# Optimization experiments

Hardware: AMD Instinct MI355X
Metric: run time of the kernel (lower is better)

Reference implementation:

```python
import jax, jax.numpy as jnp
import numpy as np

D_MODEL = 1024
D_STATE = 16
D_CONV = 4
EXPAND = 2
MLP_EXPAND = 2
D_INNER = EXPAND * D_MODEL          # 2048
DT_RANK = (D_MODEL + 15) // 16      # 64
BATCH, SEQ = 2, 1024


def setup_inputs() -> dict:
    key = jax.random.key(0)
    ks = jax.random.split(key, 16)
    s = 0.02
    inp = {
        "x": jax.random.normal(ks[0], (BATCH, SEQ, D_MODEL), jnp.float32),
        "norm1_g": jnp.ones((D_MODEL,), jnp.float32),
        "norm1_b": jnp.zeros((D_MODEL,), jnp.float32),
        "in_proj_w": jax.random.normal(ks[1], (2 * D_INNER, D_MODEL), jnp.float32) * s,
        "conv_w": jax.random.normal(ks[2], (D_INNER, 1, D_CONV), jnp.float32) * s,
        "conv_b": jnp.zeros((D_INNER,), jnp.float32),
        "x_proj_w": jax.random.normal(ks[3], (DT_RANK + 2 * D_STATE, D_INNER), jnp.float32) * s,
        "dt_proj_w": jax.random.normal(ks[4], (D_INNER, DT_RANK), jnp.float32) * s,
        "dt_proj_b": jax.random.normal(ks[5], (D_INNER,), jnp.float32) * 0.1,
        "A_log": jnp.log(jnp.broadcast_to(jnp.arange(1, D_STATE + 1, dtype=jnp.float32), (D_INNER, D_STATE))),
        "D_param": jnp.ones((D_INNER,), jnp.float32),
        "out_proj_w": jax.random.normal(ks[6], (D_MODEL, D_INNER), jnp.float32) * s,
        "norm2_g": jnp.ones((D_MODEL,), jnp.float32),
        "norm2_b": jnp.zeros((D_MODEL,), jnp.float32),
        "mlp_w1": jax.random.normal(ks[7], (MLP_EXPAND * D_MODEL, D_MODEL), jnp.float32) * s,
        "mlp_b1": jnp.zeros((MLP_EXPAND * D_MODEL,), jnp.float32),
        "mlp_w2": jax.random.normal(ks[8], (D_MODEL, MLP_EXPAND * D_MODEL), jnp.float32) * s,
        "mlp_b2": jnp.zeros((D_MODEL,), jnp.float32),
    }
    return inp


def _layernorm(x, g, b, eps=1e-5):
    m = jnp.mean(x, axis=-1, keepdims=True)
    v = jnp.var(x, axis=-1, keepdims=True)
    return (x - m) * jax.lax.rsqrt(v + eps) * g + b


def _silu(x):
    return x * jax.nn.sigmoid(x)


def _mamba(x, in_proj_w, conv_w, conv_b, x_proj_w, dt_proj_w, dt_proj_b, A_log, D_param, out_proj_w):
    # x: (B, L, d_model)
    xz = x @ in_proj_w.T                              # (B, L, 2*Di)
    xc, z = jnp.split(xz, 2, axis=-1)                 # each (B, L, Di)
    # causal depthwise conv over time
    xc_t = xc.transpose(0, 2, 1)                      # (B, Di, L)
    xc_t = jax.lax.conv_general_dilated(
        xc_t, conv_w, window_strides=(1,), padding=[(D_CONV - 1, 0)],
        dimension_numbers=("NCH", "OIH", "NCH"), feature_group_count=D_INNER,
    ) + conv_b[None, :, None]
    xc = _silu(xc_t).transpose(0, 2, 1)               # (B, L, Di)

    dbc = xc @ x_proj_w.T                             # (B, L, dt_rank + 2N)
    dt, Bm, Cm = jnp.split(dbc, [DT_RANK, DT_RANK + D_STATE], axis=-1)
    dt = jax.nn.softplus(dt @ dt_proj_w.T + dt_proj_b)  # (B, L, Di)
    A = -jnp.exp(A_log)                               # (Di, N)

    def step(h, inp):
        dt_t, B_t, C_t, x_t = inp                     # (B,Di),(B,N),(B,N),(B,Di)
        dA = jnp.exp(dt_t[..., None] * A)             # (B, Di, N)
        h = dA * h + (dt_t * x_t)[..., None] * B_t[:, None, :]
        y = jnp.einsum("bdn,bn->bd", h, C_t)
        return h, y

    h0 = jnp.zeros((x.shape[0], D_INNER, D_STATE), x.dtype)
    xs = (dt.transpose(1, 0, 2), Bm.transpose(1, 0, 2), Cm.transpose(1, 0, 2), xc.transpose(1, 0, 2))
    _, ys = jax.lax.scan(step, h0, xs)                # ys: (L, B, Di)
    y = ys.transpose(1, 0, 2) + xc * D_param          # skip term D*x
    y = y * _silu(z)
    return y @ out_proj_w.T                           # (B, L, d_model)


def reference(x, norm1_g, norm1_b, in_proj_w, conv_w, conv_b, x_proj_w, dt_proj_w,
              dt_proj_b, A_log, D_param, out_proj_w, norm2_g, norm2_b,
              mlp_w1, mlp_b1, mlp_w2, mlp_b2):
    # residual + Mamba(LN(x))  (droppath=0 -> identity)
    h = x + _mamba(_layernorm(x, norm1_g, norm1_b), in_proj_w, conv_w, conv_b,
                   x_proj_w, dt_proj_w, dt_proj_b, A_log, D_param, out_proj_w)
    # residual + MLP(LN(h))    (dropout eval -> identity)
    m = _layernorm(h, norm2_g, norm2_b)
    m = jax.nn.gelu(m @ mlp_w1.T + mlp_b1, approximate=False) @ mlp_w2.T + mlp_b2
    return h + m
```

## Files before the change

### kernel.cpp

```cpp
#include <hip/hip_runtime.h>
#include <math.h>

#define D_MODEL 1024
#define D_INNER 2048
#define DT_RANK 64
#define D_STATE 16
#define NBC 96
#define BATCH 2
#define SEQ 1024
#define TOK (BATCH*SEQ)
#define CS 32
#define NCH 32
#define XKSPLIT 16

typedef __attribute__((ext_vector_type(8))) short short8;
typedef __attribute__((ext_vector_type(4))) float f32x4;
typedef __attribute__((ext_vector_type(4))) unsigned short us4;

__device__ __forceinline__ float softplus_f(float x) {
    return (x > 20.0f) ? x : log1pf(__expf(x));
}
__device__ __forceinline__ float gelu_f(float x) {
    return 0.5f * x * (1.0f + erff(x * 0.70710678118654752f));
}
__device__ __forceinline__ float silu_f(float x) {
    return x / (1.0f + __expf(-x));
}
__device__ __forceinline__ ushort f2bf(float f) {
    unsigned u = __float_as_uint(f);
    unsigned r = (u + 0x7fffu + ((u >> 16) & 1u)) >> 16;
    return (ushort)r;
}
__device__ __forceinline__ float bf2f(ushort u) {
    return __uint_as_float(((unsigned)u) << 16);
}

__global__ void prep_kernel(const float* __restrict__ x, const float* __restrict__ g,
                            const float* __restrict__ b, ushort* __restrict__ ln_out,
                            const float* __restrict__ Wp, const float* __restrict__ Wo,
                            const float* __restrict__ W1, const float* __restrict__ W2,
                            const float* __restrict__ Wx, const float* __restrict__ Wdt,
                            ushort* __restrict__ Wpb, ushort* __restrict__ Wob,
                            ushort* __restrict__ W1b, ushort* __restrict__ W2b,
                            ushort* __restrict__ Wxb, ushort* __restrict__ Wdtb) {
    int tid = threadIdx.x;
    if (blockIdx.x < TOK) {
        int row = blockIdx.x;
        const float* xr = x + (size_t)row * D_MODEL;
        ushort* outr = ln_out + (size_t)row * D_MODEL;
        float4 v = ((const float4*)xr)[tid];
        float s  = v.x + v.y + v.z + v.w;
        float sq = v.x*v.x + v.y*v.y + v.z*v.z + v.w*v.w;
        #pragma unroll
        for (int o = 32; o > 0; o >>= 1) {
            s  += __shfl_down(s,  o);
            sq += __shfl_down(sq, o);
        }
        __shared__ float ss[4], ssq[4];
        int wid = tid >> 6, lane = tid & 63;
        if (lane == 0) { ss[wid] = s; ssq[wid] = sq; }
        __syncthreads();
        if (tid == 0) {
            float a = 0.f, c = 0.f;
            for (int i = 0; i < 4; i++) { a += ss[i]; c += ssq[i]; }
            ss[0] = a; ssq[0] = c;
        }
        __syncthreads();
        float mean = ss[0] * (1.0f / D_MODEL);
        float var  = ssq[0] * (1.0f / D_MODEL) - mean * mean;
        float rstd = rsqrtf(var + 1e-5f);
        float4 gg = ((const float4*)g)[tid];
        float4 bb = ((const float4*)b)[tid];
        ushort4 o;
        o.x = f2bf((v.x - mean) * rstd * gg.x + bb.x);
        o.y = f2bf((v.y - mean) * rstd * gg.y + bb.y);
        o.z = f2bf((v.z - mean) * rstd * gg.z + bb.z);
        o.w = f2bf((v.w - mean) * rstd * gg.w + bb.w);
        ((ushort4*)outr)[tid] = o;
        return;
    }
    int i = (blockIdx.x - TOK) * 256 + tid;
    const float* src; ushort* dst; int off;
    if      (i < 1048576) { src = Wp;  dst = Wpb;  off = i; }
    else if (i < 1572864) { src = Wo;  dst = Wob;  off = i - 1048576; }
    else if (i < 2097152) { src = W1;  dst = W1b;  off = i - 1572864; }
    else if (i < 2621440) { src = W2;  dst = W2b;  off = i - 2097152; }
    else if (i < 2670592) { src = Wx;  dst = Wxb;  off = i - 2621440; }
    else if (i < 2703360) { src = Wdt; dst = Wdtb; off = i - 2670592; }
    else return;
    float4 v = ((const float4*)src)[off];
    ushort4 o;
    o.x = f2bf(v.x); o.y = f2bf(v.y); o.z = f2bf(v.z); o.w = f2bf(v.w);
    ((ushort4*)dst)[off] = o;
}

__global__ void ln_bf16_kernel(const float* __restrict__ x, const float* __restrict__ g,
                               const float* __restrict__ b, ushort* __restrict__ out) {
    int row = blockIdx.x;
    const float* xr = x + (size_t)row * D_MODEL;
    ushort* outr = out + (size_t)row * D_MODEL;
    int tid = threadIdx.x;
    float4 v = ((const float4*)xr)[tid];
    float s  = v.x + v.y + v.z + v.w;
    float sq = v.x*v.x + v.y*v.y + v.z*v.z + v.w*v.w;
    #pragma unroll
    for (int o = 32; o > 0; o >>= 1) {
        s  += __shfl_down(s,  o);
        sq += __shfl_down(sq, o);
    }
    __shared__ float ss[4], ssq[4];
    int wid = tid >> 6, lane = tid & 63;
    if (lane == 0) { ss[wid] = s; ssq[wid] = sq; }
    __syncthreads();
    if (tid == 0) {
        float a = 0.f, c = 0.f;
        for (int i = 0; i < 4; i++) { a += ss[i]; c += ssq[i]; }
        ss[0] = a; ssq[0] = c;
    }
    __syncthreads();
    float mean = ss[0] * (1.0f / D_MODEL);
    float var  = ssq[0] * (1.0f / D_MODEL) - mean * mean;
    float rstd = rsqrtf(var + 1e-5f);
    float4 gg = ((const float4*)g)[tid];
    float4 bb = ((const float4*)b)[tid];
    ushort4 o;
    o.x = f2bf((v.x - mean) * rstd * gg.x + bb.x);
    o.y = f2bf((v.y - mean) * rstd * gg.y + bb.y);
    o.z = f2bf((v.z - mean) * rstd * gg.z + bb.z);
    o.w = f2bf((v.w - mean) * rstd * gg.w + bb.w);
    ((ushort4*)outr)[tid] = o;
}

template<int BM, int BN, int ACT, bool BIAS, bool RES, bool OUTBF>
__global__ __launch_bounds__(256)
void mfma_gemm(const ushort* __restrict__ A, const ushort* __restrict__ W,
               const float* __restrict__ bias,
               const float* __restrict__ res, int ldr,
               void* __restrict__ Cout, int ldc, int K) {
    constexpr int WM = BM / 2, WN = BN / 2, FM = WM / 16, FN = WN / 16;
    __shared__ __align__(16) ushort As[2][BM * 32];
    __shared__ __align__(16) ushort Ws[2][BN * 32];
    const int tid  = threadIdx.x;
    const int lane = tid & 63, w = tid >> 6;
    const int wr = w >> 1, wc = w & 1;
    const int row0 = blockIdx.y * BM, col0 = blockIdx.x * BN;
    const int l16 = lane >> 4, l15 = lane & 15;
    const int srow = tid >> 2;
    const int scol = (tid & 3) * 8;
    const int nk = K / 32;

    f32x4 acc[FM][FN] = {};

    auto stage = [&](int kk, int buf) {
        const int k0 = kk * 32;
        #pragma unroll
        for (int s = 0; s < BM / 64; s++) {
            const ushort* g = A + (size_t)(row0 + s * 64 + srow) * K + k0 + scol;
            __builtin_amdgcn_global_load_lds(
                (const __attribute__((address_space(1))) void*)g,
                (__attribute__((address_space(3))) void*)((char*)&As[buf][0] + s * 4096 + w * 1024),
                16, 0, 0);
        }
        #pragma unroll
        for (int s = 0; s < BN / 64; s++) {
            const ushort* g = W + (size_t)(col0 + s * 64 + srow) * K + k0 + scol;
            __builtin_amdgcn_global_load_lds(
                (const __attribute__((address_space(1))) void*)g,
                (__attribute__((address_space(3))) void*)((char*)&Ws[buf][0] + s * 4096 + w * 1024),
                16, 0, 0);
        }
    };

    stage(0, 0);
    __syncthreads();

    for (int kk = 0; kk < nk; kk++) {
        const int cur = kk & 1;
        if (kk + 1 < nk) stage(kk + 1, cur ^ 1);

        short8 a[FM], b[FN];
        #pragma unroll
        for (int m = 0; m < FM; m++)
            a[m] = *(const short8*)(&As[cur][0] + (wr * WM + m * 16 + l15) * 32 + l16 * 8);
        #pragma unroll
        for (int n = 0; n < FN; n++)
            b[n] = *(const short8*)(&Ws[cur][0] + (wc * WN + n * 16 + l15) * 32 + l16 * 8);
        #pragma unroll
        for (int m = 0; m < FM; m++)
            #pragma unroll
            for (int n = 0; n < FN; n++)
                acc[m][n] = __builtin_amdgcn_mfma_f32_16x16x32_bf16(a[m], b[n], acc[m][n], 0, 0, 0);
        __syncthreads();
    }

    #pragma unroll
    for (int m = 0; m < FM; m++) {
        const int r0 = row0 + wr * WM + m * 16 + l16 * 4;
        #pragma unroll
        for (int n = 0; n < FN; n++) {
            const int c = col0 + wc * WN + n * 16 + l15;
            const float bv = BIAS ? bias[c] : 0.f;
            #pragma unroll
            for (int q = 0; q < 4; q++) {
                const int r = r0 + q;
                float v = acc[m][n][q] + bv;
                if (ACT == 1) v = softplus_f(v);
                else if (ACT == 2) v = gelu_f(v);
                if (RES) v += res[(size_t)r * ldr + c];
                if (OUTBF) ((ushort*)Cout)[(size_t)r * ldc + c] = f2bf(v);
                else       ((float*)Cout)[(size_t)r * ldc + c] = v;
            }
        }
    }
}

__global__ __launch_bounds__(256)
void xproj_split_kernel(const ushort* __restrict__ A,
                        const ushort* __restrict__ W,
                        float* __restrict__ part) {
    __shared__ __align__(16) ushort As[2][128 * 64];
    __shared__ __align__(16) ushort Bs[2][96 * 64];
    const int tid = threadIdx.x;
    const int lane = tid & 63, w = tid >> 6;
    const int l16 = lane >> 4, l15 = lane & 15;
    const int kbase = blockIdx.x * (D_INNER / XKSPLIT);
    const int row0 = blockIdx.y * 128;
    const int srow = tid >> 3;
    const int scol = (tid & 7) * 8;

    f32x4 acc[2][6] = {};

    auto stage = [&](int k0, int buf) {
        #pragma unroll
        for (int s = 0; s < 4; s++) {
            const ushort* g = A + (size_t)(row0 + s * 32 + srow) * D_INNER + kbase + k0 + scol;
            __builtin_amdgcn_global_load_lds(
                (const __attribute__((address_space(1))) void*)g,
                (__attribute__((address_space(3))) void*)((char*)&As[buf][0] + s * 4096 + w * 1024),
                16, 0, 0);
        }
        #pragma unroll
        for (int s = 0; s < 3; s++) {
            const ushort* g = W + (size_t)(s * 32 + srow) * D_INNER + kbase + k0 + scol;
            __builtin_amdgcn_global_load_lds(
                (const __attribute__((address_space(1))) void*)g,
                (__attribute__((address_space(3))) void*)((char*)&Bs[buf][0] + s * 4096 + w * 1024),
                16, 0, 0);
        }
    };

    stage(0, 0);
    __syncthreads();

    const int nk = (D_INNER / XKSPLIT) / 64;
    for (int kk = 0; kk < nk; kk++) {
        const int cur = kk & 1;
        if (kk + 1 < nk) stage((kk + 1) * 64, cur ^ 1);
        #pragma unroll
        for (int ks = 0; ks < 2; ks++) {
            short8 a[2], b[6];
            #pragma unroll
            for (int m = 0; m < 2; m++)
                a[m] = *(const short8*)(&As[cur][0] + (w * 32 + m * 16 + l15) * 64 + ks * 32 + l16 * 8);
            #pragma unroll
            for (int n = 0; n < 6; n++)
                b[n] = *(const short8*)(&Bs[cur][0] + (n * 16 + l15) * 64 + ks * 32 + l16 * 8);
            #pragma unroll
            for (int m = 0; m < 2; m++)
                #pragma unroll
                for (int n = 0; n < 6; n++)
                    acc[m][n] = __builtin_amdgcn_mfma_f32_16x16x32_bf16(a[m], b[n], acc[m][n], 0, 0, 0);
        }
        __syncthreads();
    }

    float* p = part + (size_t)blockIdx.x * D_INNER * NBC;
    #pragma unroll
    for (int m = 0; m < 2; m++) {
        const int r0 = row0 + w * 32 + m * 16 + l16 * 4;
        #pragma unroll
        for (int n = 0; n < 6; n++) {
            const int c = n * 16 + l15;
            #pragma unroll
            for (int q = 0; q < 4; q++)
                p[(size_t)(r0 + q) * NBC + c] = acc[m][n][q];
        }
    }
}

__global__ void xproj_reduce_kernel(const float* __restrict__ part,
                                    float* __restrict__ dbc, ushort* __restrict__ dtin_b) {
    int i = blockIdx.x * 256 + threadIdx.x;
    if (i >= D_INNER * NBC) return;
    float s = 0.f;
    #pragma unroll
    for (int k = 0; k < XKSPLIT; k++) s += part[(size_t)k * D_INNER * NBC + i];
    dbc[i] = s;
    int r = i / NBC, c = i - r * NBC;
    if (c < DT_RANK) dtin_b[r * DT_RANK + c] = f2bf(s);
}

__global__ void conv_silu_kernel(const ushort* __restrict__ xzb, const float* __restrict__ cw,
                                 const float* __restrict__ cb, ushort* __restrict__ xcb) {
    int idx = blockIdx.x * 256 + threadIdx.x;
    int c  = idx & (D_INNER - 1);
    int bt = idx >> 11;
    int b  = bt >> 10;
    int t  = bt & (SEQ - 1);
    float acc = cb[c];
    #pragma unroll
    for (int j = 0; j < 4; j++) {
        int tt = t - 3 + j;
        if (tt >= 0) acc += cw[c*4 + j] * bf2f(xzb[((size_t)(b*SEQ + tt)) * 4096 + c]);
    }
    xcb[idx] = f2bf(silu_f(acc));
}

__global__ __launch_bounds__(256)
void scan_chunk_kernel(const ushort* __restrict__ dtb, const float* __restrict__ dbc,
                       const ushort* __restrict__ xcb, const float* __restrict__ A_log,
                       float* __restrict__ chunkA, float* __restrict__ chunkH) {
    __shared__ ushort dtS[64][36];
    __shared__ ushort xS[64][36];
    __shared__ float  BS[16][36];
    const int bid = blockIdx.x;
    const int dg = bid & 31, cc = (bid >> 5) & 31, b = bid >> 10;
    const int d0 = dg * 64;
    const int tid = threadIdx.x, lane = tid & 63, wv = tid >> 6;
    const int rbase = b * SEQ + cc * CS;

    #pragma unroll
    for (int k = 0; k < 8; k++) {
        int tt = k * 4 + wv;
        size_t row = (size_t)(rbase + tt);
        dtS[lane][tt] = dtb[row * D_INNER + d0 + lane];
        xS[lane][tt]  = xcb[row * D_INNER + d0 + lane];
    }
    #pragma unroll
    for (int k = 0; k < 2; k++) {
        int ii = k * 256 + tid;
        int val = ii & 15, tt = ii >> 4;
        BS[val][tt] = dbc[(size_t)(rbase + tt) * NBC + DT_RANK + val];
    }
    __syncthreads();

    const int d_local = tid >> 2, ng = tid & 3, nb = ng * 4;
    const int d = d0 + d_local;
    float Arow[4];
    #pragma unroll
    for (int j = 0; j < 4; j++) Arow[j] = -__expf(A_log[d * D_STATE + nb + j]);
    float h[4] = {};
    float ap[4] = {1.f, 1.f, 1.f, 1.f};
    #pragma unroll
    for (int it = 0; it < 8; ++it) {
        us4 dtu = *(const us4*)&dtS[d_local][it * 4];
        us4 xu  = *(const us4*)&xS[d_local][it * 4];
        f32x4 Bv[4];
        #pragma unroll
        for (int j = 0; j < 4; j++) Bv[j] = *(const f32x4*)&BS[nb + j][it * 4];
        #pragma unroll
        for (int q = 0; q < 4; ++q) {
            float dtv = bf2f(dtu[q]);
            float dtx = dtv * bf2f(xu[q]);
            #pragma unroll
            for (int j = 0; j < 4; j++) {
                float dA = __expf(dtv * Arow[j]);
                ap[j] *= dA;
                h[j] = dA * h[j] + dtx * Bv[j][q];
            }
        }
    }
    size_t obase = ((size_t)((b * NCH + cc) * D_INNER) + d) * D_STATE + nb;
    f32x4 av, hv;
    #pragma unroll
    for (int j = 0; j < 4; j++) { av[j] = ap[j]; hv[j] = h[j]; }
    *(f32x4*)&chunkA[obase] = av;
    *(f32x4*)&chunkH[obase] = hv;
}

__global__ __launch_bounds__(256)
void scan_final_kernel(const ushort* __restrict__ dtb, const float* __restrict__ dbc,
                       const ushort* __restrict__ xcb, const float* __restrict__ A_log,
                       const float* __restrict__ chunkA, const float* __restrict__ chunkH,
                       const ushort* __restrict__ xzb,
                       const float* __restrict__ Dp, ushort* __restrict__ yb) {
    __shared__ ushort dtS[64][36];
    __shared__ ushort xS[64][36];
    __shared__ ushort zS[64][36];
    __shared__ float  BS[16][36];
    __shared__ float  CSld[16][36];
    __shared__ ushort ySt[64][36];
    const int bid = blockIdx.x;
    const int dg = bid & 31, cc = (bid >> 5) & 31, b = bid >> 10;
    const int d0 = dg * 64;
    const int tid = threadIdx.x, lane = tid & 63, wv = tid >> 6;
    const int rbase = b * SEQ + cc * CS;

    #pragma unroll
    for (int k = 0; k < 8; k++) {
        int tt = k * 4 + wv;
        size_t row = (size_t)(rbase + tt);
        dtS[lane][tt] = dtb[row * D_INNER + d0 + lane];
        xS[lane][tt]  = xcb[row * D_INNER + d0 + lane];
        zS[lane][tt]  = xzb[row * 4096 + 2048 + d0 + lane];
    }
    #pragma unroll
    for (int k = 0; k < 4; k++) {
        int ii = k * 256 + tid;
        int val = ii & 31, tt = ii >> 5;
        float v = dbc[(size_t)(rbase + tt) * NBC + DT_RANK + val];
        if (val < 16) BS[val][tt] = v;
        else          CSld[val - 16][tt] = v;
    }

    const int d_local = tid >> 2, ng = tid & 3, nb = ng * 4;
    const int d = d0 + d_local;

    f32x4 hv = {0.f, 0.f, 0.f, 0.f};
    #pragma unroll 4
    for (int c = 0; c < cc; ++c) {
        size_t off = ((size_t)((b * NCH + c) * D_INNER) + d) * D_STATE + nb;
        f32x4 a  = *(const f32x4*)&chunkA[off];
        f32x4 hl = *(const f32x4*)&chunkH[off];
        hv = a * hv + hl;
    }
    float Arow[4];
    #pragma unroll
    for (int j = 0; j < 4; j++) Arow[j] = -__expf(A_log[d * D_STATE + nb + j]);
    float h[4];
    #pragma unroll
    for (int j = 0; j < 4; j++) h[j] = hv[j];
    const float Dpv = Dp[d];
    __syncthreads();

    #pragma unroll
    for (int it = 0; it < 8; ++it) {
        us4 dtu = *(const us4*)&dtS[d_local][it * 4];
        us4 xu  = *(const us4*)&xS[d_local][it * 4];
        f32x4 Bv[4], Cv[4];
        #pragma unroll
        for (int j = 0; j < 4; j++) {
            Bv[j] = *(const f32x4*)&BS[nb + j][it * 4];
            Cv[j] = *(const f32x4*)&CSld[nb + j][it * 4];
        }
        float yv4[4];
        #pragma unroll
        for (int q = 0; q < 4; ++q) {
            float dtv = bf2f(dtu[q]);
            float dtx = dtv * bf2f(xu[q]);
            float yv = 0.f;
            #pragma unroll
            for (int j = 0; j < 4; j++) {
                float dA = __expf(dtv * Arow[j]);
                h[j] = dA * h[j] + dtx * Bv[j][q];
                yv += h[j] * Cv[j][q];
            }
            yv4[q] = yv;
        }
        #pragma unroll
        for (int q = 0; q < 4; ++q) {
            yv4[q] += __shfl_xor(yv4[q], 1);
            yv4[q] += __shfl_xor(yv4[q], 2);
        }
        if (ng == 0) {
            us4 zu = *(const us4*)&zS[d_local][it * 4];
            us4 xo = *(const us4*)&xS[d_local][it * 4];
            us4 o;
            #pragma unroll
            for (int q = 0; q < 4; ++q) {
                float z = bf2f(zu[q]);
                o[q] = f2bf((yv4[q] + bf2f(xo[q]) * Dpv) * silu_f(z));
            }
            *(us4*)&ySt[d_local][it * 4] = o;
        }
    }
    __syncthreads();
    #pragma unroll
    for (int k = 0; k < 8; k++) {
        int tt = k * 4 + wv;
        yb[(size_t)(rbase + tt) * D_INNER + d0 + lane] = ySt[lane][tt];
    }
}

extern "C" void kernel_launch(void* const* d_in, const int* in_sizes, int n_in,
                              void* d_out, int out_size, void* d_ws, size_t ws_size,
                              hipStream_t stream) {
    const float* x    = (const float*)d_in[0];
    const float* n1g  = (const float*)d_in[1];
    const float* n1b  = (const float*)d_in[2];
    const float* Wp   = (const float*)d_in[3];
    const float* cw   = (const float*)d_in[4];
    const float* cb   = (const float*)d_in[5];
    const float* Wx   = (const float*)d_in[6];
    const float* Wdt  = (const float*)d_in[7];
    const float* bdt  = (const float*)d_in[8];
    const float* Alog = (const float*)d_in[9];
    const float* Dp   = (const float*)d_in[10];
    const float* Wo   = (const float*)d_in[11];
    const float* n2g  = (const float*)d_in[12];
    const float* n2b  = (const float*)d_in[13];
    const float* W1   = (const float*)d_in[14];
    const float* b1   = (const float*)d_in[15];
    const float* W2   = (const float*)d_in[16];
    const float* b2   = (const float*)d_in[17];
    float* out = (float*)d_out;
    float* ws  = (float*)d_ws;

    const size_t M1 = 1024 * 1024;
    ushort* xzb   = (ushort*)ws;
    ushort* xcb   = (ushort*)(ws + 8*M1);
    ushort* dtb_b = (ushort*)(ws + 10*M1);
    float*  part  = ws + 14*M1;
    float*  hbuf  = ws + 14*M1;
    float*  dbc   = ws + 18*M1;
    ushort* dtin_b= (ushort*)(ws + 18*M1 + 262144);
    ushort* xnb   = (ushort*)(ws + 18*M1 + 524288);
    ushort* mb    = xnb;
    ushort* yb    = (ushort*)(ws + 20*M1);
    ushort* t1b   = yb;
    ushort* Wpb   = (ushort*)(ws + 22*M1);
    float*  chunkA= ws + 22*M1;
    ushort* Wob   = (ushort*)(ws + 24*M1);
    ushort* W1b   = (ushort*)(ws + 25*M1);
    ushort* W2b   = (ushort*)(ws + 26*M1);
    ushort* Wxb   = (ushort*)(ws + 27*M1);
    ushort* Wdtb  = (ushort*)(ws + 27*M1 + 131072);
    float*  chunkH = out;

    prep_kernel<<<TOK + (2703360 + 255)/256, 256, 0, stream>>>(
        x, n1g, n1b, xnb, Wp, Wo, W1, W2, Wx, Wdt, Wpb, Wob, W1b, W2b, Wxb, Wdtb);

    mfma_gemm<128,128,0,false,false,true><<<dim3(4096/128, 2048/128), 256, 0, stream>>>(
        xnb, Wpb, nullptr, nullptr, 0, xzb, 2*D_INNER, D_MODEL);
    conv_silu_kernel<<<TOK*D_INNER/256, 256, 0, stream>>>(xzb, cw, cb, xcb);
    xproj_split_kernel<<<dim3(XKSPLIT, 2048/128), 256, 0, stream>>>(xcb, Wxb, part);
    xproj_reduce_kernel<<<(D_INNER*NBC + 255)/256, 256, 0, stream>>>(part, dbc, dtin_b);
    mfma_gemm<64,128,1,true,false,true><<<dim3(2048/128, 2048/64), 256, 0, stream>>>(
        dtin_b, Wdtb, bdt, nullptr, 0, dtb_b, D_INNER, DT_RANK);
    scan_chunk_kernel<<<BATCH*NCH*(D_INNER/64), 256, 0, stream>>>(dtb_b, dbc, xcb, Alog, chunkA, chunkH);
    scan_final_kernel<<<BATCH*NCH*(D_INNER/64), 256, 0, stream>>>(dtb_b, dbc, xcb, Alog,
                                                                  chunkA, chunkH, xzb, Dp, yb);
    mfma_gemm<64,64,0,false,true,false><<<dim3(1024/64, 2048/64), 256, 0, stream>>>(
        yb, Wob, nullptr, x, D_MODEL, hbuf, D_MODEL, D_INNER);
    ln_bf16_kernel<<<TOK, 256, 0, stream>>>(hbuf, n2g, n2b, mb);
    mfma_gemm<64,128,2,true,false,true><<<dim3(2048/128, 2048/64), 256, 0, stream>>>(
        mb, W1b, b1, nullptr, 0, t1b, D_INNER, D_MODEL);
    mfma_gemm<64,64,0,true,true,false><<<dim3(1024/64, 2048/64), 256, 0, stream>>>(
        t1b, W2b, b2, hbuf, D_MODEL, out, D_MODEL, D_INNER);
}
```

Baseline: 225.2 us.

## Fuse chunked scan passes into one cooperative kernel with grid sync

Merges the chunk-local scan and the final scan into a single cooperative kernel. A grid-wide barrier separates writing the per-chunk decay products and states from the prefix combine, so dt, x, B and z are loaded into shared memory once instead of twice and one launch is removed. The output staging buffer now reuses the z tile to save LDS. The cooperative launch needs all 2048 blocks resident at once (launch bounds request 8 blocks per CU), and the grid barrier adds its own cost. If residency cannot be met, the launch fails.

```diff
diff --git a/kernel.cpp b/kernel.cpp
--- a/kernel.cpp
+++ b/kernel.cpp
@@ -1,5 +1,8 @@
 #include <hip/hip_runtime.h>
+#include <hip/hip_cooperative_groups.h>
 #include <math.h>
+
+namespace cg = cooperative_groups;
 
 #define D_MODEL 1024
 #define D_INNER 2048
@@ -316,72 +319,10 @@
     xcb[idx] = f2bf(silu_f(acc));
 }
 
-__global__ __launch_bounds__(256)
-void scan_chunk_kernel(const ushort* __restrict__ dtb, const float* __restrict__ dbc,
+__global__ __launch_bounds__(256, 8)
+void scan_fused_kernel(const ushort* __restrict__ dtb, const float* __restrict__ dbc,
                        const ushort* __restrict__ xcb, const float* __restrict__ A_log,
-                       float* __restrict__ chunkA, float* __restrict__ chunkH) {
-    __shared__ ushort dtS[64][36];
-    __shared__ ushort xS[64][36];
-    __shared__ float  BS[16][36];
-    const int bid = blockIdx.x;
-    const int dg = bid & 31, cc = (bid >> 5) & 31, b = bid >> 10;
-    const int d0 = dg * 64;
-    const int tid = threadIdx.x, lane = tid & 63, wv = tid >> 6;
-    const int rbase = b * SEQ + cc * CS;
-
-    #pragma unroll
-    for (int k = 0; k < 8; k++) {
-        int tt = k * 4 + wv;
-        size_t row = (size_t)(rbase + tt);
-        dtS[lane][tt] = dtb[row * D_INNER + d0 + lane];
-        xS[lane][tt]  = xcb[row * D_INNER + d0 + lane];
-    }
-    #pragma unroll
-    for (int k = 0; k < 2; k++) {
-        int ii = k * 256 + tid;
-        int val = ii & 15, tt = ii >> 4;
-        BS[val][tt] = dbc[(size_t)(rbase + tt) * NBC + DT_RANK + val];
-    }
-    __syncthreads();
-
-    const int d_local = tid >> 2, ng = tid & 3, nb = ng * 4;
-    const int d = d0 + d_local;
-    float Arow[4];
-    #pragma unroll
-    for (int j = 0; j < 4; j++) Arow[j] = -__expf(A_log[d * D_STATE + nb + j]);
-    float h[4] = {};
-    float ap[4] = {1.f, 1.f, 1.f, 1.f};
-    #pragma unroll
-    for (int it = 0; it < 8; ++it) {
-        us4 dtu = *(const us4*)&dtS[d_local][it * 4];
-        us4 xu  = *(const us4*)&xS[d_local][it * 4];
-        f32x4 Bv[4];
-        #pragma unroll
-        for (int j = 0; j < 4; j++) Bv[j] = *(const f32x4*)&BS[nb + j][it * 4];
-        #pragma unroll
-        for (int q = 0; q < 4; ++q) {
-            float dtv = bf2f(dtu[q]);
-            float dtx = dtv * bf2f(xu[q]);
-            #pragma unroll
-            for (int j = 0; j < 4; j++) {
-                float dA = __expf(dtv * Arow[j]);
-                ap[j] *= dA;
-                h[j] = dA * h[j] + dtx * Bv[j][q];
-            }
-        }
-    }
-    size_t obase = ((size_t)((b * NCH + cc) * D_INNER) + d) * D_STATE + nb;
-    f32x4 av, hv;
-    #pragma unroll
-    for (int j = 0; j < 4; j++) { av[j] = ap[j]; hv[j] = h[j]; }
-    *(f32x4*)&chunkA[obase] = av;
-    *(f32x4*)&chunkH[obase] = hv;
-}
-
-__global__ __launch_bounds__(256)
-void scan_final_kernel(const ushort* __restrict__ dtb, const float* __restrict__ dbc,
-                       const ushort* __restrict__ xcb, const float* __restrict__ A_log,
-                       const float* __restrict__ chunkA, const float* __restrict__ chunkH,
+                       float* __restrict__ chunkA, float* __restrict__ chunkH,
                        const ushort* __restrict__ xzb,
                        const float* __restrict__ Dp, ushort* __restrict__ yb) {
     __shared__ ushort dtS[64][36];
@@ -389,7 +330,6 @@
     __shared__ ushort zS[64][36];
     __shared__ float  BS[16][36];
     __shared__ float  CSld[16][36];
-    __shared__ ushort ySt[64][36];
     const int bid = blockIdx.x;
     const int dg = bid & 31, cc = (bid >> 5) & 31, b = bid >> 10;
     const int d0 = dg * 64;
@@ -412,26 +352,56 @@
         if (val < 16) BS[val][tt] = v;
         else          CSld[val - 16][tt] = v;
     }
+    __syncthreads();
 
     const int d_local = tid >> 2, ng = tid & 3, nb = ng * 4;
     const int d = d0 + d_local;
+    float Arow[4];
+    #pragma unroll
+    for (int j = 0; j < 4; j++) Arow[j] = -__expf(A_log[d * D_STATE + nb + j]);
+
+    float h[4] = {};
+    float ap[4] = {1.f, 1.f, 1.f, 1.f};
+    #pragma unroll
+    for (int it = 0; it < 8; ++it) {
+        us4 dtu = *(const us4*)&dtS[d_local][it * 4];
+        us4 xu  = *(const us4*)&xS[d_local][it * 4];
+        f32x4 Bv[4];
+        #pragma unroll
+        for (int j = 0; j < 4; j++) Bv[j] = *(const f32x4*)&BS[nb + j][it * 4];
+        #pragma unroll
+        for (int q = 0; q < 4; ++q) {
+            float dtv = bf2f(dtu[q]);
+            float dtx = dtv * bf2f(xu[q]);
+            #pragma unroll
+            for (int j = 0; j < 4; j++) {
+                float dA = __expf(dtv * Arow[j]);
+                ap[j] *= dA;
+                h[j] = dA * h[j] + dtx * Bv[j][q];
+            }
+        }
+    }
+    size_t obase = ((size_t)((b * NCH + cc) * D_INNER) + d) * D_STATE + nb;
+    {
+        f32x4 av, hv;
+        #pragma unroll
+        for (int j = 0; j < 4; j++) { av[j] = ap[j]; hv[j] = h[j]; }
+        *(f32x4*)&chunkA[obase] = av;
+        *(f32x4*)&chunkH[obase] = hv;
+    }
+    __threadfence();
+    cg::this_grid().sync();
 
     f32x4 hv = {0.f, 0.f, 0.f, 0.f};
-    #pragma unroll 4
     for (int c = 0; c < cc; ++c) {
         size_t off = ((size_t)((b * NCH + c) * D_INNER) + d) * D_STATE + nb;
         f32x4 a  = *(const f32x4*)&chunkA[off];
         f32x4 hl = *(const f32x4*)&chunkH[off];
         hv = a * hv + hl;
     }
-    float Arow[4];
-    #pragma unroll
-    for (int j = 0; j < 4; j++) Arow[j] = -__expf(A_log[d * D_STATE + nb + j]);
-    float h[4];
     #pragma unroll
     for (int j = 0; j < 4; j++) h[j] = hv[j];
     const float Dpv = Dp[d];
-    __syncthreads();
 
     #pragma unroll
     for (int it = 0; it < 8; ++it) {
@@ -471,14 +441,14 @@
                 float z = bf2f(zu[q]);
                 o[q] = f2bf((yv4[q] + bf2f(xo[q]) * Dpv) * silu_f(z));
             }
-            *(us4*)&ySt[d_local][it * 4] = o;
+            *(us4*)&zS[d_local][it * 4] = o;
         }
     }
     __syncthreads();
     #pragma unroll
     for (int k = 0; k < 8; k++) {
         int tt = k * 4 + wv;
-        yb[(size_t)(rbase + tt) * D_INNER + d0 + lane] = ySt[lane][tt];
+        yb[(size_t)(rbase + tt) * D_INNER + d0 + lane] = zS[lane][tt];
     }
 }
 
@@ -537,9 +507,15 @@
     xproj_reduce_kernel<<<(D_INNER*NBC + 255)/256, 256, 0, stream>>>(part, dbc, dtin_b);
     mfma_gemm<64,128,1,true,false,true><<<dim3(2048/128, 2048/64), 256, 0, stream>>>(
         dtin_b, Wdtb, bdt, nullptr, 0, dtb_b, D_INNER, DT_RANK);
-    scan_chunk_kernel<<<BATCH*NCH*(D_INNER/64), 256, 0, stream>>>(dtb_b, dbc, xcb, Alog, chunkA, chunkH);
-    scan_final_kernel<<<BATCH*NCH*(D_INNER/64), 256, 0, stream>>>(dtb_b, dbc, xcb, Alog,
-                                                                  chunkA, chunkH, xzb, Dp, yb);
+    {
+        const ushort* a0 = dtb_b; const float* a1 = dbc; const ushort* a2 = xcb;
+        const float* a3 = Alog; float* a4 = chunkA; float* a5 = chunkH;
+        const ushort* a6 = xzb; const float* a7 = Dp; ushort* a8 = yb;
+        void* args[] = {&a0, &a1, &a2, &a3, &a4, &a5, &a6, &a7, &a8};
+        hipLaunchCooperativeKernel((void*)scan_fused_kernel,
+                                   dim3(BATCH * NCH * (D_INNER / 64)), dim3(256),
+                                   args, 0, stream);
+    }
     mfma_gemm<64,64,0,false,true,false><<<dim3(1024/64, 2048/64), 256, 0, stream>>>(
         yb, Wob, nullptr, x, D_MODEL, hbuf, D_MODEL, D_INNER);
     ln_bf16_kernel<<<TOK, 256, 0, stream>>>(hbuf, n2g, n2b, mb);
```

Result: slower. 873.3 us (+287.8%).

## Precompute chunk prefix states in a separate combine kernel for scan

Applied to the files above, without the earlier changes.

Adds a scan_combine kernel that walks the 32 chunk summaries once per (batch, channel, state) and writes each chunk's incoming state in place into chunkH. Before this, every scan_final block redid a prefix loop over all earlier chunks, which costs quadratic loads overall. scan_final now loads a single precomputed state, reuses the zS shared buffer to stage its output so it can drop one LDS array, and asks for higher occupancy through launch bounds. The trade-off is one extra kernel launch and a serial 32-step loop per thread in the combine kernel.

```diff
diff --git a/kernel.cpp b/kernel.cpp
--- a/kernel.cpp
+++ b/kernel.cpp
@@ -378,18 +378,33 @@
     *(f32x4*)&chunkH[obase] = hv;
 }
 
-__global__ __launch_bounds__(256)
+__global__ void scan_combine_kernel(const float* __restrict__ chunkA, float* __restrict__ chunkH) {
+    int idx = blockIdx.x * 256 + threadIdx.x;
+    int n = idx & (D_STATE - 1);
+    int dn = idx >> 4;
+    int d = dn & (D_INNER - 1);
+    int b = dn >> 11;
+    float h = 0.f;
+    #pragma unroll 4
+    for (int c = 0; c < NCH; c++) {
+        size_t o = ((size_t)((b * NCH + c) * D_INNER) + d) * D_STATE + n;
+        float a  = chunkA[o];
+        float hl = chunkH[o];
+        chunkH[o] = h;
+        h = a * h + hl;
+    }
+}
+
+__global__ __launch_bounds__(256, 8)
 void scan_final_kernel(const ushort* __restrict__ dtb, const float* __restrict__ dbc,
                        const ushort* __restrict__ xcb, const float* __restrict__ A_log,
-                       const float* __restrict__ chunkA, const float* __restrict__ chunkH,
-                       const ushort* __restrict__ xzb,
+                       const float* __restrict__ chunkH, const ushort* __restrict__ xzb,
                        const float* __restrict__ Dp, ushort* __restrict__ yb) {
     __shared__ ushort dtS[64][36];
     __shared__ ushort xS[64][36];
     __shared__ ushort zS[64][36];
     __shared__ float  BS[16][36];
     __shared__ float  CSld[16][36];
-    __shared__ ushort ySt[64][36];
     const int bid = blockIdx.x;
     const int dg = bid & 31, cc = (bid >> 5) & 31, b = bid >> 10;
     const int d0 = dg * 64;
@@ -412,26 +427,19 @@
         if (val < 16) BS[val][tt] = v;
         else          CSld[val - 16][tt] = v;
     }
+    __syncthreads();
 
     const int d_local = tid >> 2, ng = tid & 3, nb = ng * 4;
     const int d = d0 + d_local;
-
-    f32x4 hv = {0.f, 0.f, 0.f, 0.f};
-    #pragma unroll 4
-    for (int c = 0; c < cc; ++c) {
-        size_t off = ((size_t)((b * NCH + c) * D_INNER) + d) * D_STATE + nb;
-        f32x4 a  = *(const f32x4*)&chunkA[off];
-        f32x4 hl = *(const f32x4*)&chunkH[off];
-        hv = a * hv + hl;
-    }
     float Arow[4];
     #pragma unroll
     for (int j = 0; j < 4; j++) Arow[j] = -__expf(A_log[d * D_STATE + nb + j]);
+    size_t obase = ((size_t)((b * NCH + cc) * D_INNER) + d) * D_STATE + nb;
+    f32x4 hv = *(const f32x4*)&chunkH[obase];
     float h[4];
     #pragma unroll
     for (int j = 0; j < 4; j++) h[j] = hv[j];
     const float Dpv = Dp[d];
-    __syncthreads();
 
     #pragma unroll
     for (int it = 0; it < 8; ++it) {
@@ -471,14 +479,14 @@
                 float z = bf2f(zu[q]);
                 o[q] = f2bf((yv4[q] + bf2f(xo[q]) * Dpv) * silu_f(z));
             }
-            *(us4*)&ySt[d_local][it * 4] = o;
+            *(us4*)&zS[d_local][it * 4] = o;
         }
     }
     __syncthreads();
     #pragma unroll
     for (int k = 0; k < 8; k++) {
         int tt = k * 4 + wv;
-        yb[(size_t)(rbase + tt) * D_INNER + d0 + lane] = ySt[lane][tt];
+        yb[(size_t)(rbase + tt) * D_INNER + d0 + lane] = zS[lane][tt];
     }
 }
 
@@ -538,8 +546,9 @@
     mfma_gemm<64,128,1,true,false,true><<<dim3(2048/128, 2048/64), 256, 0, stream>>>(
         dtin_b, Wdtb, bdt, nullptr, 0, dtb_b, D_INNER, DT_RANK);
     scan_chunk_kernel<<<BATCH*NCH*(D_INNER/64), 256, 0, stream>>>(dtb_b, dbc, xcb, Alog, chunkA, chunkH);
+    scan_combine_kernel<<<BATCH*D_INNER*D_STATE/256, 256, 0, stream>>>(chunkA, chunkH);
     scan_final_kernel<<<BATCH*NCH*(D_INNER/64), 256, 0, stream>>>(dtb_b, dbc, xcb, Alog,
-                                                                  chunkA, chunkH, xzb, Dp, yb);
+                                                                  chunkH, xzb, Dp, yb);
     mfma_gemm<64,64,0,false,true,false><<<dim3(1024/64, 2048/64), 256, 0, stream>>>(
         yb, Wob, nullptr, x, D_MODEL, hbuf, D_MODEL, D_INNER);
     ln_bf16_kernel<<<TOK, 256, 0, stream>>>(hbuf, n2g, n2b, mb);
```

Result: slower. 230.5 us (+2.4%).
